# Optimization experiments

Measured on AMD Instinct MI355X. Metric: run time of the kernel, lower is better.

Reference implementation:

```python
import jax, jax.numpy as jnp
import numpy as np

N = 50000       # nodes
E = 1600000     # edges (avg degree 32)
F_IN = 128      # input node features
HID = 64        # hidden_dim
H = 2           # heads in conv1
NEG_SLOPE = 0.2 # PyG GATConv default


def gat_conv(x, W, a_src, a_dst, b, src, dst, heads, out_ch):
    """PyG-style GATConv (concat=True). x:[n,f], W:[f,heads*out_ch],
    a_src/a_dst:[heads,out_ch], b:[heads*out_ch], src/dst:[e]."""
    n = x.shape[0]
    xh = (x @ W).reshape(n, heads, out_ch)              # [n,H,C]
    s_src = jnp.sum(xh * a_src[None], axis=-1)          # [n,H]
    s_dst = jnp.sum(xh * a_dst[None], axis=-1)          # [n,H]
    e = jax.nn.leaky_relu(s_src[src] + s_dst[dst], NEG_SLOPE)  # [e,H]
    # segment softmax over incoming edges of each destination node
    emax = jax.ops.segment_max(e, dst, num_segments=n)  # [n,H]
    emax = jnp.where(jnp.isfinite(emax), emax, 0.0)
    p = jnp.exp(e - emax[dst])
    denom = jax.ops.segment_sum(p, dst, num_segments=n)
    alpha = p / (denom[dst] + 1e-16)                    # [e,H]
    out = jax.ops.segment_sum(xh[src] * alpha[..., None], dst, num_segments=n)
    return out.reshape(n, heads * out_ch) + b


def setup_inputs() -> dict:
    key = jax.random.key(0)
    ks = jax.random.split(key, 14)
    g = lambda k, shape, fan: jax.random.normal(k, shape, jnp.float32) / np.sqrt(fan).astype(np.float32)
    return {
        "x": jax.random.normal(ks[0], (N, F_IN), jnp.float32),
        "edge_index": jax.random.randint(ks[1], (2, E), 0, N, jnp.int32),
        "W1": g(ks[2], (F_IN, H * HID), F_IN),
        "a_src1": g(ks[3], (H, HID), HID),
        "a_dst1": g(ks[4], (H, HID), HID),
        "b1": jnp.zeros((H * HID,), jnp.float32),
        "W2": g(ks[5], (H * HID, HID), H * HID),
        "a_src2": g(ks[6], (1, HID), HID),
        "a_dst2": g(ks[7], (1, HID), HID),
        "b2": jnp.zeros((HID,), jnp.float32),
        "Wm": g(ks[8], (HID, 1), HID),
        "bm": jnp.zeros((1,), jnp.float32),
        "Wl": g(ks[9], (HID, 4), HID),
        "bl": jnp.zeros((4,), jnp.float32),
    }


def reference(x, edge_index, W1, a_src1, a_dst1, b1, W2, a_src2, a_dst2, b2, Wm, bm, Wl, bl):
    n = x.shape[0]
    loop = jnp.arange(n, dtype=edge_index.dtype)        # PyG add_self_loops=True
    src = jnp.concatenate([edge_index[0], loop])
    dst = jnp.concatenate([edge_index[1], loop])
    h = jax.nn.relu(gat_conv(x, W1, a_src1, a_dst1, b1, src, dst, H, HID))
    # dropout layers are identity in eval mode
    h = jax.nn.relu(gat_conv(h, W2, a_src2, a_dst2, b2, src, dst, 1, HID))
    mortality = h @ Wm + bm   # [n,1]
    los = h @ Wl + bl         # [n,4]
    return (mortality, los)
```

## Files before the change

### kernel.cpp

```cpp
#include <hip/hip_runtime.h>
#include <hip/hip_bf16.h>

typedef __hip_bfloat16 bf16;
typedef __attribute__((ext_vector_type(8))) short short8;
typedef __attribute__((ext_vector_type(4))) float f32x4;

static __device__ __forceinline__ float lrelu(float x){ return x > 0.f ? x : 0.2f * x; }

static __device__ __forceinline__ float ldf(const void* p, size_t i, int f32){
  return f32 ? ((const float*)p)[i] : __bfloat162float(((const bf16*)p)[i]);
}

static __device__ __forceinline__ float wsum(float v){
#pragma unroll
  for (int o = 32; o; o >>= 1) v += __shfl_xor(v, o, 64);
  return v;
}
static __device__ __forceinline__ float qsum(float v){
  v += __shfl_xor(v, 1); v += __shfl_xor(v, 2);
  v += __shfl_xor(v, 4); v += __shfl_xor(v, 8);
  return v;
}

static __device__ __forceinline__ unsigned short f2bf(float x){
  unsigned u = __float_as_uint(x);
  unsigned r = (u + 0x7fffu + ((u >> 16) & 1u)) >> 16;
  return (unsigned short)r;
}
static __device__ __forceinline__ float bfval(unsigned short h){
  return __uint_as_float(((unsigned)h) << 16);
}
static __device__ __forceinline__ unsigned packbf2(float a, float b){
  return ((unsigned)f2bf(b) << 16) | (unsigned)f2bf(a);
}
static __device__ __forceinline__ float unlo(unsigned v){ return __uint_as_float(v << 16); }
static __device__ __forceinline__ float unhi(unsigned v){ return __uint_as_float(v & 0xffff0000u); }

#define CAP 10240
#define EPB 16
#define CHUNK (256 * EPB)
#define PREPB 96
#define SORTCAP 9216

__global__ __launch_bounds__(256) void k_prep_scatter(
    const unsigned short* __restrict__ xprobe,
    const void* __restrict__ W1, const void* __restrict__ W2,
    int* __restrict__ flag,
    unsigned short* __restrict__ w1hi, unsigned short* __restrict__ w1lo,
    unsigned short* __restrict__ w2hi, unsigned short* __restrict__ w2lo,
    const int* __restrict__ ei, int* __restrict__ bucketCur,
    unsigned* __restrict__ binned, int E, int Etot){
  __shared__ int lcnt[256];
  __shared__ int lcur[256];
  int t = threadIdx.x;
  if (blockIdx.x < PREPB){
    if (t == 0) lcnt[0] = 0;
    __syncthreads();
    int bad = 0;
    for (int i = t; i < 512; i += 256){
      int e = (xprobe[i] >> 7) & 0xFF;
      if (e >= 133) bad++;
    }
    if (bad) atomicAdd(&lcnt[0], bad);
    __syncthreads();
    const int f = lcnt[0] > 8;
    if (blockIdx.x == 0 && t == 0) *flag = f;
    int blk = blockIdx.x;
    const void* W; unsigned short *hi, *lo; int ncol, nct, tg;
    if (blk < 64){ W = W1; hi = w1hi; lo = w1lo; ncol = 128; nct = 8; tg = blk * 256 + t; }
    else         { W = W2; hi = w2hi; lo = w2lo; ncol = 64;  nct = 4; tg = (blk - 64) * 256 + t; }
    int j = tg & 7;
    int lane = (tg >> 3) & 63;
    int ct = (tg >> 9) % nct;
    int kc = tg / (512 * nct);
    int k = kc * 32 + ((lane >> 4) << 3) + j;
    int col = ct * 16 + (lane & 15);
    float w = ldf(W, (size_t)k * ncol + col, f);
    unsigned short h = f2bf(w);
    hi[tg] = h;
    lo[tg] = f2bf(w - bfval(h));
  } else {
    lcnt[t] = 0;
    __syncthreads();
    int base = (blockIdx.x - PREPB) * CHUNK;
    int vsrc[EPB], vdst[EPB];
#pragma unroll
    for (int k = 0; k < EPB; k++){
      int i = base + k * 256 + t;
      vdst[k] = -1;
      if (i < Etot){
        if (i < E){ vsrc[k] = ei[i]; vdst[k] = ei[E + i]; }
        else { vsrc[k] = i - E; vdst[k] = i - E; }
        atomicAdd(&lcnt[vdst[k] >> 8], 1);
      }
    }
    __syncthreads();
    lcur[t] = lcnt[t] ? atomicAdd(&bucketCur[t], lcnt[t]) : 0;
    __syncthreads();
#pragma unroll
    for (int k = 0; k < EPB; k++){
      if (vdst[k] >= 0){
        int b = vdst[k] >> 8;
        int p = atomicAdd(&lcur[b], 1);
        binned[(size_t)b * CAP + p] = (unsigned)vsrc[k] | ((unsigned)(vdst[k] & 255) << 24);
      }
    }
  }
}

__global__ __launch_bounds__(256) void k_sort_gemm1(
    const int* __restrict__ bucketCur, const unsigned* __restrict__ binned,
    int* __restrict__ deg, int* __restrict__ offs, int* __restrict__ csr, int nbuck,
    const void* __restrict__ x,
    const unsigned short* __restrict__ whi, const unsigned short* __restrict__ wlo,
    const void* __restrict__ a_src1, const void* __restrict__ a_dst1,
    const int* __restrict__ flagp,
    unsigned* __restrict__ xh1p, float* __restrict__ ssrc1, float* __restrict__ sdst1, int n){
  __shared__ int smem[768 + SORTCAP];
  int t = threadIdx.x;
  if ((int)blockIdx.x < nbuck){
    int* lcnt = smem;
    int* lsc  = smem + 256;
    int* lcur = smem + 512;
    int* lsrc = smem + 768;
    int b = blockIdx.x;
    int s0 = b * CAP;
    int cnt = bucketCur[b];
    int node0 = b << 8;
    lcnt[t] = 0;
    __syncthreads();
    for (int i = t; i < cnt; i += 256){
      unsigned v = binned[s0 + i];
      atomicAdd(&lcnt[v >> 24], 1);
    }
    __syncthreads();
    lsc[t] = lcnt[t];
    __syncthreads();
#pragma unroll
    for (int o = 1; o < 256; o <<= 1){
      int xv = (t >= o) ? lsc[t - o] : 0;
      __syncthreads();
      lsc[t] += xv;
      __syncthreads();
    }
    int excl = lsc[t] - lcnt[t];
    int node = node0 + t;
    if (node < n){ deg[node] = lcnt[t]; offs[node] = s0 + excl; }
    lcur[t] = excl;
    __syncthreads();
    if (cnt <= SORTCAP){
      for (int i = t; i < cnt; i += 256){
        unsigned v = binned[s0 + i];
        int p = atomicAdd(&lcur[v >> 24], 1);
        lsrc[p] = (int)(v & 0xFFFFFFu);
      }
      __syncthreads();
      for (int i = t; i < cnt; i += 256) csr[s0 + i] = lsrc[i];
    } else {
      for (int i = t; i < cnt; i += 256){
        unsigned v = binned[s0 + i];
        int p = atomicAdd(&lcur[v >> 24], 1);
        csr[s0 + p] = (int)(v & 0xFFFFFFu);
      }
    }
  } else {
    const int f = *flagp;
    int lane = t & 63, w = t >> 6;
    int c16 = lane & 15, quad = lane >> 4;
    int nbw = (blockIdx.x - nbuck) * 64 + w * 16;
    int an = min(nbw + c16, n - 1);
    f32x4 acc[8];
#pragma unroll
    for (int ct = 0; ct < 8; ct++)
#pragma unroll
      for (int r = 0; r < 4; r++) acc[ct][r] = 0.f;

#pragma unroll
    for (int kc = 0; kc < 4; kc++){
      float av[8];
      short8 ahi, alo;
      if (f){
        const float* row = (const float*)x + (size_t)an * 128 + kc * 32 + quad * 8;
        float4 v0 = *(const float4*)row;
        float4 v1 = *(const float4*)(row + 4);
        av[0] = v0.x; av[1] = v0.y; av[2] = v0.z; av[3] = v0.w;
        av[4] = v1.x; av[5] = v1.y; av[6] = v1.z; av[7] = v1.w;
#pragma unroll
        for (int j = 0; j < 8; j++){
          unsigned short h = f2bf(av[j]);
          ahi[j] = (short)h;
          alo[j] = (short)f2bf(av[j] - bfval(h));
        }
      } else {
        const unsigned short* row = (const unsigned short*)x + (size_t)an * 128 + kc * 32 + quad * 8;
        uint4 v = *(const uint4*)row;
        ahi[0] = (short)(v.x & 0xffff); ahi[1] = (short)(v.x >> 16);
        ahi[2] = (short)(v.y & 0xffff); ahi[3] = (short)(v.y >> 16);
        ahi[4] = (short)(v.z & 0xffff); ahi[5] = (short)(v.z >> 16);
        ahi[6] = (short)(v.w & 0xffff); ahi[7] = (short)(v.w >> 16);
#pragma unroll
        for (int j = 0; j < 8; j++) alo[j] = 0;
      }
#pragma unroll
      for (int ct = 0; ct < 8; ct++){
        const short8 bhi = *(const short8*)(whi + (((size_t)(kc * 8 + ct) * 64 + lane) << 3));
        const short8 blo = *(const short8*)(wlo + (((size_t)(kc * 8 + ct) * 64 + lane) << 3));
        acc[ct] = __builtin_amdgcn_mfma_f32_16x16x32_bf16(ahi, blo, acc[ct], 0, 0, 0);
        acc[ct] = __builtin_amdgcn_mfma_f32_16x16x32_bf16(alo, bhi, acc[ct], 0, 0, 0);
        acc[ct] = __builtin_amdgcn_mfma_f32_16x16x32_bf16(ahi, bhi, acc[ct], 0, 0, 0);
      }
    }

    float as[8], ad[8];
#pragma unroll
    for (int ct = 0; ct < 8; ct++){
      as[ct] = ldf(a_src1, ct * 16 + c16, f);
      ad[ct] = ldf(a_dst1, ct * 16 + c16, f);
    }
    float vs0[4], vs1[4], vd0[4], vd1[4];
#pragma unroll
    for (int r = 0; r < 4; r++){
      float s0 = 0.f, s1 = 0.f, d0 = 0.f, d1 = 0.f;
#pragma unroll
      for (int ct = 0; ct < 4; ct++){
        s0 += acc[ct][r] * as[ct];         d0 += acc[ct][r] * ad[ct];
        s1 += acc[ct + 4][r] * as[ct + 4]; d1 += acc[ct + 4][r] * ad[ct + 4];
      }
      vs0[r] = qsum(s0); vs1[r] = qsum(s1);
      vd0[r] = qsum(d0); vd1[r] = qsum(d1);
    }
#pragma unroll
    for (int r = 0; r < 4; r++){
      int node = nbw + quad * 4 + r;
      if (node < n){
#pragma unroll
        for (int ct = 0; ct < 4; ct++)
          xh1p[(size_t)node * 64 + ct * 16 + c16] = packbf2(acc[ct][r], acc[ct + 4][r]);
      }
    }
    if (c16 == 0){
#pragma unroll
      for (int r = 0; r < 4; r++){
        int node = nbw + quad * 4 + r;
        if (node < n){
          ssrc1[node * 2]     = vs0[r];
          ssrc1[node * 2 + 1] = vs1[r];
          sdst1[node * 2]     = vd0[r];
          sdst1[node * 2 + 1] = vd1[r];
        }
      }
    }
  }
}

__global__ __launch_bounds__(256) void k_gemm2m(
    const float* __restrict__ h1,
    const unsigned short* __restrict__ whi, const unsigned short* __restrict__ wlo,
    const void* __restrict__ a_src2, const void* __restrict__ a_dst2,
    const int* __restrict__ flagp,
    unsigned short* __restrict__ xh2b, float* __restrict__ ssrc2, float* __restrict__ sdst2, int n){
  const int f = *flagp;
  int t = threadIdx.x;
  int lane = t & 63, w = t >> 6;
  int c16 = lane & 15, quad = lane >> 4;
  int nbw = blockIdx.x * 64 + w * 16;
  int an = min(nbw + c16, n - 1);
  f32x4 acc[4];
#pragma unroll
  for (int ct = 0; ct < 4; ct++)
#pragma unroll
    for (int r = 0; r < 4; r++) acc[ct][r] = 0.f;

#pragma unroll
  for (int kc = 0; kc < 4; kc++){
    const float* row = h1 + (size_t)an * 128 + kc * 32 + quad * 8;
    float4 v0 = *(const float4*)row;
    float4 v1 = *(const float4*)(row + 4);
    float av[8] = {v0.x, v0.y, v0.z, v0.w, v1.x, v1.y, v1.z, v1.w};
    short8 ahi, alo;
#pragma unroll
    for (int j = 0; j < 8; j++){
      unsigned short h = f2bf(av[j]);
      ahi[j] = (short)h;
      alo[j] = (short)f2bf(av[j] - bfval(h));
    }
#pragma unroll
    for (int ct = 0; ct < 4; ct++){
      const short8 bhi = *(const short8*)(whi + (((size_t)(kc * 4 + ct) * 64 + lane) << 3));
      const short8 blo = *(const short8*)(wlo + (((size_t)(kc * 4 + ct) * 64 + lane) << 3));
      acc[ct] = __builtin_amdgcn_mfma_f32_16x16x32_bf16(ahi, blo, acc[ct], 0, 0, 0);
      acc[ct] = __builtin_amdgcn_mfma_f32_16x16x32_bf16(alo, bhi, acc[ct], 0, 0, 0);
      acc[ct] = __builtin_amdgcn_mfma_f32_16x16x32_bf16(ahi, bhi, acc[ct], 0, 0, 0);
    }
  }

  float as[4], ad[4];
#pragma unroll
  for (int ct = 0; ct < 4; ct++){
    as[ct] = ldf(a_src2, ct * 16 + c16, f);
    ad[ct] = ldf(a_dst2, ct * 16 + c16, f);
  }
  float vs[4], vd[4];
#pragma unroll
  for (int r = 0; r < 4; r++){
    float s = 0.f, d = 0.f;
#pragma unroll
    for (int ct = 0; ct < 4; ct++){
      s += acc[ct][r] * as[ct];
      d += acc[ct][r] * ad[ct];
    }
    vs[r] = qsum(s); vd[r] = qsum(d);
  }
#pragma unroll
  for (int r = 0; r < 4; r++){
    int node = nbw + quad * 4 + r;
    if (node < n){
#pragma unroll
      for (int ct = 0; ct < 4; ct++)
        xh2b[(size_t)node * 64 + ct * 16 + c16] = f2bf(acc[ct][r]);
    }
  }
  if (c16 == 0){
#pragma unroll
    for (int r = 0; r < 4; r++){
      int node = nbw + quad * 4 + r;
      if (node < n){ ssrc2[node] = vs[r]; sdst2[node] = vd[r]; }
    }
  }
}

__global__ __launch_bounds__(256) void k_agg1(
    const int* __restrict__ offs, const int* __restrict__ deg, const int* __restrict__ csr,
    const float2* __restrict__ ssrc, const float2* __restrict__ sdst,
    const unsigned* __restrict__ xh1p, const void* __restrict__ b1,
    const int* __restrict__ flagp, float* __restrict__ h1, int n){
  int wid = (int)(((size_t)blockIdx.x * blockDim.x + threadIdx.x) >> 6);
  int lane = threadIdx.x & 63;
  if (wid >= n) return;
  int st = offs[wid], d = deg[wid];
  int half = lane >> 5, u = lane & 31;
  float2 sd = sdst[wid];
  const uint2* xp = (const uint2*)xh1p;
  float Z0l = 0.f, Z1l = 0.f;
  float a0x = 0.f, a0y = 0.f, a1x = 0.f, a1y = 0.f;
  for (int base = 0; base < d; base += 64){
    int idx = base + lane;
    bool val = idx < d;
    int s = csr[st + (val ? idx : 0)];
    float2 sv = ssrc[s];
    float e0 = fminf(lrelu(sv.x + sd.x), 80.f);
    float e1 = fminf(lrelu(sv.y + sd.y), 80.f);
    float p0 = val ? __expf(e0) : 0.f;
    float p1 = val ? __expf(e1) : 0.f;
    Z0l += p0; Z1l += p1;
    int cnt = min(64, d - base);
    int pairs = (cnt + 1) >> 1;
    for (int pj = 0; pj < pairs; pj += 8){
      int sj[8]; float q0v[8], q1v[8]; uint2 vv[8];
#pragma unroll
      for (int k = 0; k < 8; k++){
        int jj = ((pj + k) << 1) + half;
        sj[k] = __shfl(s, jj);
        q0v[k] = __shfl(p0, jj);
        q1v[k] = __shfl(p1, jj);
      }
#pragma unroll
      for (int k = 0; k < 8; k++)
        vv[k] = xp[(size_t)(unsigned)sj[k] * 32 + u];
#pragma unroll
      for (int k = 0; k < 8; k++){
        a0x = fmaf(q0v[k], unlo(vv[k].x), a0x); a0y = fmaf(q0v[k], unlo(vv[k].y), a0y);
        a1x = fmaf(q1v[k], unhi(vv[k].x), a1x); a1y = fmaf(q1v[k], unhi(vv[k].y), a1y);
      }
    }
  }
  a0x += __shfl_xor(a0x, 32); a0y += __shfl_xor(a0y, 32);
  a1x += __shfl_xor(a1x, 32); a1y += __shfl_xor(a1y, 32);
  float Z0 = wsum(Z0l), Z1 = wsum(Z1l);
  const int f = *flagp;
  float Zh = half ? Z1 : Z0;
  float ax = half ? a1x : a0x;
  float ay = half ? a1y : a0y;
  float inv = 1.f / (Zh + 1e-16f);
  float bx = ldf(b1, half * 64 + 2 * u, f);
  float by = ldf(b1, half * 64 + 2 * u + 1, f);
  float2 o;
  o.x = fmaxf(ax * inv + bx, 0.f);
  o.y = fmaxf(ay * inv + by, 0.f);
  *(float2*)&h1[(size_t)wid * 128 + half * 64 + 2 * u] = o;
}

__global__ __launch_bounds__(256) void k_agg2(
    const int* __restrict__ offs, const int* __restrict__ deg, const int* __restrict__ csr,
    const float* __restrict__ ssrc, const float* __restrict__ sdstA,
    const unsigned short* __restrict__ xh2b, const void* __restrict__ bias2,
    const void* __restrict__ Wm, const void* __restrict__ bm,
    const void* __restrict__ Wlos, const void* __restrict__ bl,
    const int* __restrict__ flagp, void* __restrict__ out, int n){
  int wid = (int)(((size_t)blockIdx.x * blockDim.x + threadIdx.x) >> 6);
  int lane = threadIdx.x & 63;
  if (wid >= n) return;
  int st = offs[wid], d = deg[wid];
  int half = lane >> 5, u = lane & 31;
  float sd = sdstA[wid];
  const unsigned* xp = (const unsigned*)xh2b;
  float Zl = 0.f, ax = 0.f, ay = 0.f;
  for (int base = 0; base < d; base += 64){
    int idx = base + lane;
    bool val = idx < d;
    int s = csr[st + (val ? idx : 0)];
    float e = fminf(lrelu(ssrc[s] + sd), 80.f);
    float p = val ? __expf(e) : 0.f;
    Zl += p;
    int cnt = min(64, d - base);
    int pairs = (cnt + 1) >> 1;
    for (int pj = 0; pj < pairs; pj += 8){
      int sj[8]; float qv[8]; unsigned vv[8];
#pragma unroll
      for (int k = 0; k < 8; k++){
        int jj = ((pj + k) << 1) + half;
        sj[k] = __shfl(s, jj);
        qv[k] = __shfl(p, jj);
      }
#pragma unroll
      for (int k = 0; k < 8; k++)
        vv[k] = xp[(size_t)(unsigned)sj[k] * 32 + u];
#pragma unroll
      for (int k = 0; k < 8; k++){
        ax = fmaf(qv[k], unlo(vv[k]), ax);
        ay = fmaf(qv[k], unhi(vv[k]), ay);
      }
    }
  }
  ax += __shfl_xor(ax, 32);
  ay += __shfl_xor(ay, 32);
  float Z = wsum(Zl);
  const int f = *flagp;
  float inv = 1.f / (Z + 1e-16f);
  float hx = fmaxf(ax * inv + ldf(bias2, 2 * u, f), 0.f);
  float hy = fmaxf(ay * inv + ldf(bias2, 2 * u + 1, f), 0.f);
  bool lo32 = (half == 0);
  float mo = wsum(lo32 ? hx * ldf(Wm, 2 * u, f) + hy * ldf(Wm, 2 * u + 1, f) : 0.f);
  float l0 = wsum(lo32 ? hx * ldf(Wlos, (2 * u) * 4 + 0, f) + hy * ldf(Wlos, (2 * u + 1) * 4 + 0, f) : 0.f);
  float l1 = wsum(lo32 ? hx * ldf(Wlos, (2 * u) * 4 + 1, f) + hy * ldf(Wlos, (2 * u + 1) * 4 + 1, f) : 0.f);
  float l2 = wsum(lo32 ? hx * ldf(Wlos, (2 * u) * 4 + 2, f) + hy * ldf(Wlos, (2 * u + 1) * 4 + 2, f) : 0.f);
  float l3 = wsum(lo32 ? hx * ldf(Wlos, (2 * u) * 4 + 3, f) + hy * ldf(Wlos, (2 * u + 1) * 4 + 3, f) : 0.f);
  if (lane == 0){
    float vm = mo + ldf(bm, 0, f);
    float v0 = l0 + ldf(bl, 0, f);
    float v1 = l1 + ldf(bl, 1, f);
    float v2 = l2 + ldf(bl, 2, f);
    float v3 = l3 + ldf(bl, 3, f);
    if (f){
      float* o = (float*)out;
      o[wid] = vm;
      float4 lv = make_float4(v0, v1, v2, v3);
      *(float4*)&o[n + wid * 4] = lv;
    } else {
      bf16* o = (bf16*)out;
      o[wid] = __float2bfloat16(vm);
      o[n + wid * 4 + 0] = __float2bfloat16(v0); o[n + wid * 4 + 1] = __float2bfloat16(v1);
      o[n + wid * 4 + 2] = __float2bfloat16(v2); o[n + wid * 4 + 3] = __float2bfloat16(v3);
    }
  }
}

extern "C" void kernel_launch(void* const* d_in, const int* in_sizes, int n_in,
                              void* d_out, int out_size, void* d_ws, size_t ws_size,
                              hipStream_t stream){
  const void* x      = d_in[0];
  const int*  ei     = (const int*)d_in[1];
  const void* W1     = d_in[2];
  const void* a_src1 = d_in[3];
  const void* a_dst1 = d_in[4];
  const void* b1     = d_in[5];
  const void* W2     = d_in[6];
  const void* a_src2 = d_in[7];
  const void* a_dst2 = d_in[8];
  const void* bias2  = d_in[9];
  const void* Wm     = d_in[10];
  const void* bm     = d_in[11];
  const void* Wlos   = d_in[12];
  const void* bl     = d_in[13];

  const int N = in_sizes[0] / 128;
  const int E = in_sizes[1] / 2;
  const int Etot = E + N;
  const int NBUCK = (N + 255) >> 8;

  char* base = (char*)d_ws;
  size_t off = 0;
  auto alloc = [&](size_t bytes) -> void* {
    void* r = base + off;
    off += (bytes + 255) & ~(size_t)255;
    return r;
  };
  int*      flag  = (int*)alloc(256);
  unsigned* xh1p  = (unsigned*)alloc((size_t)N * 64 * 4);
  float*    h1    = (float*)alloc((size_t)N * 128 * 4);
  float*    ssrc1 = (float*)alloc((size_t)N * 2 * 4);
  float*    sdst1 = (float*)alloc((size_t)N * 2 * 4);
  float*    ssrc2 = (float*)alloc((size_t)N * 4);
  float*    sdst2 = (float*)alloc((size_t)N * 4);
  int*      deg    = (int*)alloc((size_t)N * 4);
  int*      offsb  = (int*)alloc((size_t)N * 4);
  unsigned* binned = (unsigned*)alloc((size_t)NBUCK * CAP * 4);
  int*      csr    = (int*)alloc((size_t)NBUCK * CAP * 4);
  int*      bucketCur = (int*)alloc(1024);
  unsigned short* w1hi = (unsigned short*)alloc(16384 * 2);
  unsigned short* w1lo = (unsigned short*)alloc(16384 * 2);
  unsigned short* w2hi = (unsigned short*)alloc(8192 * 2);
  unsigned short* w2lo = (unsigned short*)alloc(8192 * 2);
  unsigned short* xh2b = (unsigned short*)xh1p;

  const int nchunk = (Etot + CHUNK - 1) / CHUNK;
  const int ngemm1 = (N + 63) / 64;

  hipMemsetAsync(bucketCur, 0, (size_t)NBUCK * 4, stream);

  k_prep_scatter<<<PREPB + nchunk, 256, 0, stream>>>(
      (const unsigned short*)x, W1, W2, flag, w1hi, w1lo, w2hi, w2lo,
      ei, bucketCur, binned, E, Etot);

  k_sort_gemm1<<<NBUCK + ngemm1, 256, 0, stream>>>(
      bucketCur, binned, deg, offsb, csr, NBUCK,
      x, w1hi, w1lo, a_src1, a_dst1, flag, xh1p, ssrc1, sdst1, N);

  k_agg1<<<(N + 3) / 4, 256, 0, stream>>>(offsb, deg, csr, (const float2*)ssrc1, (const float2*)sdst1,
                                          xh1p, b1, flag, h1, N);

  k_gemm2m<<<(N + 63) / 64, 256, 0, stream>>>(h1, w2hi, w2lo, a_src2, a_dst2, flag, xh2b, ssrc2, sdst2, N);
  k_agg2<<<(N + 3) / 4, 256, 0, stream>>>(offsb, deg, csr, ssrc2, sdst2, xh2b, bias2,
                                          Wm, bm, Wlos, bl, flag, d_out, N);
}
```

Baseline: 262.8 us.

## Store layer-1 output as bf16 and broadcast edge data via LDS

```diff
diff --git a/kernel.cpp b/kernel.cpp
--- a/kernel.cpp
+++ b/kernel.cpp
@@ -254,7 +254,7 @@
 }
 
 __global__ __launch_bounds__(256) void k_gemm2m(
-    const float* __restrict__ h1,
+    const unsigned* __restrict__ h1p,
     const unsigned short* __restrict__ whi, const unsigned short* __restrict__ wlo,
     const void* __restrict__ a_src2, const void* __restrict__ a_dst2,
     const int* __restrict__ flagp,
@@ -273,23 +273,18 @@
 
 #pragma unroll
   for (int kc = 0; kc < 4; kc++){
-    const float* row = h1 + (size_t)an * 128 + kc * 32 + quad * 8;
-    float4 v0 = *(const float4*)row;
-    float4 v1 = *(const float4*)(row + 4);
-    float av[8] = {v0.x, v0.y, v0.z, v0.w, v1.x, v1.y, v1.z, v1.w};
-    short8 ahi, alo;
-#pragma unroll
-    for (int j = 0; j < 8; j++){
-      unsigned short h = f2bf(av[j]);
-      ahi[j] = (short)h;
-      alo[j] = (short)f2bf(av[j] - bfval(h));
-    }
+    const uint4* hp = (const uint4*)h1p;
+    uint4 v = hp[(size_t)an * 16 + kc * 4 + quad];
+    short8 ahi;
+    ahi[0] = (short)(v.x & 0xffff); ahi[1] = (short)(v.x >> 16);
+    ahi[2] = (short)(v.y & 0xffff); ahi[3] = (short)(v.y >> 16);
+    ahi[4] = (short)(v.z & 0xffff); ahi[5] = (short)(v.z >> 16);
+    ahi[6] = (short)(v.w & 0xffff); ahi[7] = (short)(v.w >> 16);
 #pragma unroll
     for (int ct = 0; ct < 4; ct++){
       const short8 bhi = *(const short8*)(whi + (((size_t)(kc * 4 + ct) * 64 + lane) << 3));
       const short8 blo = *(const short8*)(wlo + (((size_t)(kc * 4 + ct) * 64 + lane) << 3));
       acc[ct] = __builtin_amdgcn_mfma_f32_16x16x32_bf16(ahi, blo, acc[ct], 0, 0, 0);
-      acc[ct] = __builtin_amdgcn_mfma_f32_16x16x32_bf16(alo, bhi, acc[ct], 0, 0, 0);
       acc[ct] = __builtin_amdgcn_mfma_f32_16x16x32_bf16(ahi, bhi, acc[ct], 0, 0, 0);
     }
   }
@@ -333,7 +328,9 @@
     const int* __restrict__ offs, const int* __restrict__ deg, const int* __restrict__ csr,
     const float2* __restrict__ ssrc, const float2* __restrict__ sdst,
     const unsigned* __restrict__ xh1p, const void* __restrict__ b1,
-    const int* __restrict__ flagp, float* __restrict__ h1, int n){
+    const int* __restrict__ flagp, unsigned* __restrict__ h1p, int n){
+  __shared__ float4 stg[4][64];
+  int wv = threadIdx.x >> 6;
   int wid = (int)(((size_t)blockIdx.x * blockDim.x + threadIdx.x) >> 6);
   int lane = threadIdx.x & 63;
   if (wid >= n) return;
@@ -353,6 +350,8 @@
     float p0 = val ? __expf(e0) : 0.f;
     float p1 = val ? __expf(e1) : 0.f;
     Z0l += p0; Z1l += p1;
+    float4 tv; tv.x = __uint_as_float((unsigned)s); tv.y = p0; tv.z = p1; tv.w = 0.f;
+    stg[wv][lane] = tv;
     int cnt = min(64, d - base);
     int pairs = (cnt + 1) >> 1;
     for (int pj = 0; pj < pairs; pj += 8){
@@ -360,9 +359,10 @@
 #pragma unroll
       for (int k = 0; k < 8; k++){
         int jj = ((pj + k) << 1) + half;
-        sj[k] = __shfl(s, jj);
-        q0v[k] = __shfl(p0, jj);
-        q1v[k] = __shfl(p1, jj);
+        float4 v = stg[wv][jj];
+        sj[k] = (int)__float_as_uint(v.x);
+        q0v[k] = v.y;
+        q1v[k] = v.z;
       }
 #pragma unroll
       for (int k = 0; k < 8; k++)
@@ -384,10 +384,9 @@
   float inv = 1.f / (Zh + 1e-16f);
   float bx = ldf(b1, half * 64 + 2 * u, f);
   float by = ldf(b1, half * 64 + 2 * u + 1, f);
-  float2 o;
-  o.x = fmaxf(ax * inv + bx, 0.f);
-  o.y = fmaxf(ay * inv + by, 0.f);
-  *(float2*)&h1[(size_t)wid * 128 + half * 64 + 2 * u] = o;
+  float ox = fmaxf(ax * inv + bx, 0.f);
+  float oy = fmaxf(ay * inv + by, 0.f);
+  h1p[(size_t)wid * 64 + half * 32 + u] = packbf2(ox, oy);
 }
 
 __global__ __launch_bounds__(256) void k_agg2(
@@ -397,6 +396,8 @@
     const void* __restrict__ Wm, const void* __restrict__ bm,
     const void* __restrict__ Wlos, const void* __restrict__ bl,
     const int* __restrict__ flagp, void* __restrict__ out, int n){
+  __shared__ float2 stg[4][64];
+  int wv = threadIdx.x >> 6;
   int wid = (int)(((size_t)blockIdx.x * blockDim.x + threadIdx.x) >> 6);
   int lane = threadIdx.x & 63;
   if (wid >= n) return;
@@ -412,6 +413,8 @@
     float e = fminf(lrelu(ssrc[s] + sd), 80.f);
     float p = val ? __expf(e) : 0.f;
     Zl += p;
+    float2 tv; tv.x = __uint_as_float((unsigned)s); tv.y = p;
+    stg[wv][lane] = tv;
     int cnt = min(64, d - base);
     int pairs = (cnt + 1) >> 1;
     for (int pj = 0; pj < pairs; pj += 8){
@@ -419,8 +422,9 @@
 #pragma unroll
       for (int k = 0; k < 8; k++){
         int jj = ((pj + k) << 1) + half;
-        sj[k] = __shfl(s, jj);
-        qv[k] = __shfl(p, jj);
+        float2 v = stg[wv][jj];
+        sj[k] = (int)__float_as_uint(v.x);
+        qv[k] = v.y;
       }
 #pragma unroll
       for (int k = 0; k < 8; k++)
@@ -497,7 +501,7 @@
   };
   int*      flag  = (int*)alloc(256);
   unsigned* xh1p  = (unsigned*)alloc((size_t)N * 64 * 4);
-  float*    h1    = (float*)alloc((size_t)N * 128 * 4);
+  unsigned* h1p   = (unsigned*)alloc((size_t)N * 64 * 4);
   float*    ssrc1 = (float*)alloc((size_t)N * 2 * 4);
   float*    sdst1 = (float*)alloc((size_t)N * 2 * 4);
   float*    ssrc2 = (float*)alloc((size_t)N * 4);
@@ -527,9 +531,9 @@
       x, w1hi, w1lo, a_src1, a_dst1, flag, xh1p, ssrc1, sdst1, N);
 
   k_agg1<<<(N + 3) / 4, 256, 0, stream>>>(offsb, deg, csr, (const float2*)ssrc1, (const float2*)sdst1,
-                                          xh1p, b1, flag, h1, N);
-
-  k_gemm2m<<<(N + 63) / 64, 256, 0, stream>>>(h1, w2hi, w2lo, a_src2, a_dst2, flag, xh2b, ssrc2, sdst2, N);
+                                          xh1p, b1, flag, h1p, N);
+
+  k_gemm2m<<<(N + 63) / 64, 256, 0, stream>>>(h1p, w2hi, w2lo, a_src2, a_dst2, flag, xh2b, ssrc2, sdst2, N);
   k_agg2<<<(N + 3) / 4, 256, 0, stream>>>(offsb, deg, csr, ssrc2, sdst2, xh2b, bias2,
                                           Wm, bm, Wlos, bl, flag, d_out, N);
 }
```

Result: faster. 257.0 us (-2.2%).
